# Optimization experiments

Hardware: AMD Instinct MI355X
Metric: run time of the kernel (lower is better)

## Reference

```python
import jax, jax.numpy as jnp
import numpy as np

B, T, D, H = 2, 2048, 1024, 16
HD = D // H
ALPHA = HD ** -0.5
EPS = 1e-5


def setup_inputs() -> dict:
    key = jax.random.key(0)
    ks = jax.random.split(key, 8)
    x = jax.random.normal(ks[0], (B, T, D), dtype=jnp.float32)
    # additive causal mask: 0 where allowed, -inf where disallowed
    causal = jnp.triu(jnp.ones((T, T), dtype=bool), k=1)
    attention_mask = jnp.where(causal, -jnp.inf, 0.0).astype(jnp.float32)
    rab = jax.random.normal(ks[1], (1, H, T, T), dtype=jnp.float32) * 0.02
    W_in = jax.random.normal(ks[2], (D, 4 * D), dtype=jnp.float32) * (D ** -0.5)
    b_in = jnp.zeros((4 * D,), dtype=jnp.float32)
    W_out = jax.random.normal(ks[3], (D, D), dtype=jnp.float32) * (D ** -0.5)
    b_out = jnp.zeros((D,), dtype=jnp.float32)
    ln_w = jnp.ones((D,), dtype=jnp.float32)
    ln_b = jnp.zeros((D,), dtype=jnp.float32)
    return {"x": x, "attention_mask": attention_mask, "rab": rab,
            "W_in": W_in, "b_in": b_in, "W_out": W_out, "b_out": b_out,
            "ln_w": ln_w, "ln_b": ln_b}


def _heads(t):  # [B,T,D] -> [B,H,T,HD]
    return t.reshape(B, T, H, HD).transpose(0, 2, 1, 3)


def _layernorm(t, w, b):
    mu = jnp.mean(t, axis=-1, keepdims=True)
    var = jnp.mean(jnp.square(t - mu), axis=-1, keepdims=True)
    return (t - mu) * jax.lax.rsqrt(var + EPS) * w + b


def reference(x, attention_mask, rab, W_in, b_in, W_out, b_out, ln_w, ln_b):
    h = jax.nn.silu(x @ W_in + b_in)                      # [B,T,4D]
    U, V, Q, K = jnp.split(h, 4, axis=-1)
    Qh, Kh, Vh = _heads(Q), _heads(K), _heads(V)
    logits = jnp.einsum('bhqd,bhkd->bhqk', Qh, Kh) * ALPHA
    logits = logits + rab + attention_mask[None, None]    # [B,H,T,T]
    # allowed counts from the additive mask (0 == allowed)
    allowed = (attention_mask == 0).astype(jnp.float32)   # [T,T]
    denom = jnp.clip(jnp.sum(allowed, axis=-1, keepdims=True), 1.0)  # [T,1]
    logits_safe = jnp.where(jnp.isinf(logits) & (logits < 0), -1e9, logits)
    attn = jax.nn.silu(logits_safe) / denom[None, None]
    AV = jnp.einsum('bhqk,bhkd->bhqd', attn, Vh)
    AV = AV.transpose(0, 2, 1, 3).reshape(B, T, D)
    y = (_layernorm(AV, ln_w, ln_b) * U) @ W_out + b_out
    return y
```

## Files before the change

### kernel.cpp

```cpp
#include <hip/hip_runtime.h>

#define BATCH 2
#define TSEQ 2048
#define DIM 1024
#define NH 16
#define HDIM 64
#define MROWS (BATCH * TSEQ)

typedef __attribute__((ext_vector_type(4))) float f32x4;
typedef __attribute__((ext_vector_type(8))) short short8;

__device__ __forceinline__ unsigned short f2bf(float f) {
    union { float f; unsigned int u; } x; x.f = f;
    unsigned int r = x.u + 0x7fffu + ((x.u >> 16) & 1u);
    return (unsigned short)(r >> 16);
}

__device__ __forceinline__ float silu_f(float v) {
    return v * __builtin_amdgcn_rcpf(1.f + __expf(-v));
}

__device__ __forceinline__ void gl_lds16(const void* g, void* l) {
    __builtin_amdgcn_global_load_lds(
        (const __attribute__((address_space(1))) void*)g,
        (__attribute__((address_space(3))) void*)l, 16, 0, 0);
}

__device__ __forceinline__ short8 rd_swz(const unsigned short* base, int row, int chunk) {
    const char* b = (const char*)base;
    return *(const short8*)(b + row * 128 + (((chunk ^ (row & 7)) << 4)));
}

__global__ __launch_bounds__(256) void k_convert(const float* __restrict__ in,
                                                 unsigned short* __restrict__ out,
                                                 int n4) {
    int i = blockIdx.x * 256 + threadIdx.x;
    if (i < n4) {
        float4 v = ((const float4*)in)[i];
        union { unsigned short s[4]; uint2 u; } o;
        o.s[0] = f2bf(v.x); o.s[1] = f2bf(v.y); o.s[2] = f2bf(v.z); o.s[3] = f2bf(v.w);
        ((uint2*)out)[i] = o.u;
    }
}

__global__ __launch_bounds__(256) void k_transpose(const float* __restrict__ in,
                                                   unsigned short* __restrict__ out,
                                                   int R, int C) {
    __shared__ float tile[32][33];
    int tx = threadIdx.x, ty = threadIdx.y;
    int c0 = blockIdx.x * 32, r0 = blockIdx.y * 32;
    #pragma unroll
    for (int i = 0; i < 32; i += 8)
        tile[ty + i][tx] = in[(size_t)(r0 + ty + i) * C + c0 + tx];
    __syncthreads();
    #pragma unroll
    for (int i = 0; i < 32; i += 8)
        out[(size_t)(c0 + ty + i) * R + r0 + tx] = f2bf(tile[tx][ty + i]);
}

__global__ __launch_bounds__(256) void k_transpose_bf16(const unsigned short* __restrict__ in,
                                                        unsigned short* __restrict__ out,
                                                        int R, int C) {
    __shared__ unsigned short t[64][66];
    int tx = threadIdx.x, ty = threadIdx.y;
    int c0 = blockIdx.x * 64, r0 = blockIdx.y * 64;
    #pragma unroll
    for (int i = 0; i < 64; i += 4)
        t[ty + i][tx] = in[(size_t)(r0 + ty + i) * C + c0 + tx];
    __syncthreads();
    #pragma unroll
    for (int i = 0; i < 64; i += 4)
        out[(size_t)(c0 + ty + i) * R + r0 + tx] = t[tx][ty + i];
}

template <int EPI>
__global__ __launch_bounds__(256) void k_gemm(
    const unsigned short* __restrict__ A, const unsigned short* __restrict__ Bt,
    int M, int N, int K, const float* __restrict__ bias,
    float* __restrict__ outU, unsigned short* __restrict__ outV,
    unsigned short* __restrict__ outQ, unsigned short* __restrict__ outK,
    float* __restrict__ outY)
{
    __shared__ __align__(16) unsigned short sA[128 * 32];
    __shared__ __align__(16) unsigned short sB[128 * 32];
    const int tid = threadIdx.x;
    const int bm = blockIdx.x, bn = blockIdx.y;
    const int row0 = bm * 128, col0 = bn * 128;
    const int lane = tid & 63, w = tid >> 6;
    const int wrow = (w >> 1) * 64, wcol = (w & 1) * 64;
    const int lr = lane & 15, lk = lane >> 4;

    f32x4 acc[4][4] = {};

    for (int k0 = 0; k0 < K; k0 += 32) {
        for (int c = tid; c < 512; c += 256) {
            int r = c >> 2, kc = c & 3;
            gl_lds16(A + (size_t)(row0 + r) * K + k0 + kc * 8, sA + c * 8);
            gl_lds16(Bt + (size_t)(col0 + r) * K + k0 + kc * 8, sB + c * 8);
        }
        __syncthreads();
        short8 af[4], bf[4];
        #pragma unroll
        for (int m = 0; m < 4; ++m)
            af[m] = *(const short8*)(sA + (wrow + m * 16 + lr) * 32 + lk * 8);
        #pragma unroll
        for (int n = 0; n < 4; ++n)
            bf[n] = *(const short8*)(sB + (wcol + n * 16 + lr) * 32 + lk * 8);
        #pragma unroll
        for (int m = 0; m < 4; ++m)
            #pragma unroll
            for (int n = 0; n < 4; ++n)
                acc[m][n] = __builtin_amdgcn_mfma_f32_16x16x32_bf16(af[m], bf[n], acc[m][n], 0, 0, 0);
        __syncthreads();
    }

    #pragma unroll
    for (int m = 0; m < 4; ++m) {
        #pragma unroll
        for (int n = 0; n < 4; ++n) {
            int cg = col0 + wcol + n * 16 + lr;
            float bv = bias[cg];
            #pragma unroll
            for (int j = 0; j < 4; ++j) {
                int rg = row0 + wrow + m * 16 + lk * 4 + j;
                float v = acc[m][n][j] + bv;
                if (EPI == 1) {
                    float s = silu_f(v);
                    int sec = cg >> 10, cc = cg & 1023;
                    size_t off = ((size_t)rg << 10) + cc;
                    if (sec == 0) outU[off] = s;
                    else if (sec == 1) outV[off] = f2bf(s);
                    else if (sec == 2) outQ[off] = f2bf(s * 0.125f);
                    else outK[off] = f2bf(s);
                } else {
                    outY[(size_t)rg * N + cg] = v;
                }
            }
        }
    }
}

__global__ __launch_bounds__(256, 4) void k_attn(
    const unsigned short* __restrict__ Qb,
    const unsigned short* __restrict__ Kb,
    const unsigned short* __restrict__ Vt,
    const float* __restrict__ rab,
    float* __restrict__ AV)
{
    __shared__ __align__(16) unsigned short sK[2][64 * 64];
    __shared__ __align__(16) unsigned short sVt[2][64 * 64];
    __shared__ __align__(16) unsigned short sP[64 * 64];

    const int tid = threadIdx.x;
    const int lane = tid & 63;
    const int w = tid >> 6;
    const int lr = lane & 15;
    const int lk = lane >> 4;

    const int bid = blockIdx.x;
    const int idx = bid & 255;
    const int g = bid >> 8;
    const int h = idx & 15;
    const int r_ = idx >> 4;
    const int bb = g >> 1;
    const int qt = (g & 1) ? (31 - r_) : r_;
    const int q0 = qt * 64;

    short8 qreg[2];
    #pragma unroll
    for (int ks = 0; ks < 2; ++ks)
        qreg[ks] = *(const short8*)(Qb + (((size_t)(bb * TSEQ + q0 + w * 16 + lr)) << 10)
                                     + h * 64 + ks * 32 + lk * 8);

    int qrow[4]; float invq[4];
    #pragma unroll
    for (int j = 0; j < 4; ++j) {
        qrow[j] = q0 + w * 16 + lk * 4 + j;
        invq[j] = 1.f / (float)(qrow[j] + 1);
    }

    f32x4 acc[4] = {};

    #define STAGE(buf, kt_) do {                                                      \
        int k0s = (kt_) * 64;                                                         \
        for (int c = tid; c < 512; c += 256) {                                        \
            int rr = c >> 3, kc = c & 7;                                              \
            int kcs = kc ^ (rr & 7);                                                  \
            gl_lds16(Kb + (((size_t)(bb * TSEQ + k0s + rr)) << 10) + h * 64 + kcs * 8,\
                     sK[buf] + c * 8);                                                \
            gl_lds16(Vt + (((size_t)(h * 64 + rr)) << 12) + bb * TSEQ + k0s + kcs * 8,\
                     sVt[buf] + c * 8);                                               \
        }                                                                             \
    } while (0)

    const float* rabh = rab + (size_t)h * TSEQ * TSEQ;

    STAGE(0, 0);
    float rvc[4][4];
    #pragma unroll
    for (int nt = 0; nt < 4; ++nt)
        #pragma unroll
        for (int j = 0; j < 4; ++j)
            rvc[nt][j] = rabh[(size_t)qrow[j] * TSEQ + nt * 16 + lr];
    __syncthreads();

    int cur = 0;
    for (int kt = 0; kt <= qt; ++kt) {
        const int k0 = kt * 64;
        const bool have_next = (kt < qt);
        if (have_next) STAGE(cur ^ 1, kt + 1);

        float rvn[4][4];
        if (have_next) {
            #pragma unroll
            for (int nt = 0; nt < 4; ++nt)
                #pragma unroll
                for (int j = 0; j < 4; ++j)
                    rvn[nt][j] = rabh[(size_t)qrow[j] * TSEQ + k0 + 64 + nt * 16 + lr];
        }

        f32x4 s[4] = {};
        #pragma unroll
        for (int ks = 0; ks < 2; ++ks) {
            #pragma unroll
            for (int nt = 0; nt < 4; ++nt)
                s[nt] = __builtin_amdgcn_mfma_f32_16x16x32_bf16(
                    qreg[ks], rd_swz(sK[cur], nt * 16 + lr, ks * 4 + lk), s[nt], 0, 0, 0);
        }

        const bool full = (kt < qt);
        char* pb = (char*)sP;
        #pragma unroll
        for (int nt = 0; nt < 4; ++nt) {
            int k = k0 + nt * 16 + lr;
            #pragma unroll
            for (int j = 0; j < 4; ++j) {
                int prow = w * 16 + lk * 4 + j;
                float v = s[nt][j] + rvc[nt][j];
                float pv = (full || k <= qrow[j]) ? silu_f(v) * invq[j] : 0.f;
                *(unsigned short*)(pb + prow * 128 + (((nt * 16 + lr) * 2) ^ ((prow & 7) << 4)))
                    = f2bf(pv);
            }
        }

        #pragma unroll
        for (int ks = 0; ks < 2; ++ks) {
            short8 ap = rd_swz(sP, w * 16 + lr, ks * 4 + lk);
            #pragma unroll
            for (int dt = 0; dt < 4; ++dt)
                acc[dt] = __builtin_amdgcn_mfma_f32_16x16x32_bf16(
                    ap, rd_swz(sVt[cur], dt * 16 + lr, ks * 4 + lk), acc[dt], 0, 0, 0);
        }

        if (have_next) {
            #pragma unroll
            for (int nt = 0; nt < 4; ++nt)
                #pragma unroll
                for (int j = 0; j < 4; ++j)
                    rvc[nt][j] = rvn[nt][j];
        }

        __syncthreads();
        cur ^= 1;
    }
    #undef STAGE

    #pragma unroll
    for (int dt = 0; dt < 4; ++dt)
        #pragma unroll
        for (int j = 0; j < 4; ++j)
            AV[(((size_t)(bb * TSEQ + qrow[j])) << 10) + h * 64 + dt * 16 + lr] = acc[dt][j];
}

__global__ __launch_bounds__(256) void k_ln(const float* __restrict__ AV,
                                            const float* __restrict__ U,
                                            const float* __restrict__ lnw,
                                            const float* __restrict__ lnb,
                                            unsigned short* __restrict__ z) {
    __shared__ float red[8];
    const int row = blockIdx.x, tid = threadIdx.x;
    float4 v = ((const float4*)(AV + ((size_t)row << 10)))[tid];
    float s = v.x + v.y + v.z + v.w;
    float s2 = v.x * v.x + v.y * v.y + v.z * v.z + v.w * v.w;
    #pragma unroll
    for (int o = 32; o > 0; o >>= 1) { s += __shfl_xor(s, o); s2 += __shfl_xor(s2, o); }
    const int w = tid >> 6;
    if ((tid & 63) == 0) { red[w] = s; red[4 + w] = s2; }
    __syncthreads();
    s = red[0] + red[1] + red[2] + red[3];
    s2 = red[4] + red[5] + red[6] + red[7];
    const float mu = s * (1.f / 1024.f);
    const float var = s2 * (1.f / 1024.f) - mu * mu;
    const float rstd = rsqrtf(var + 1e-5f);
    float4 uw = ((const float4*)(U + ((size_t)row << 10)))[tid];
    float4 lw = ((const float4*)lnw)[tid];
    float4 lb = ((const float4*)lnb)[tid];
    union { unsigned short o[4]; uint2 u; } ov;
    ov.o[0] = f2bf(((v.x - mu) * rstd * lw.x + lb.x) * uw.x);
    ov.o[1] = f2bf(((v.y - mu) * rstd * lw.y + lb.y) * uw.y);
    ov.o[2] = f2bf(((v.z - mu) * rstd * lw.z + lb.z) * uw.z);
    ov.o[3] = f2bf(((v.w - mu) * rstd * lw.w + lb.w) * uw.w);
    ((uint2*)z)[((size_t)row << 8) + tid] = ov.u;
}

extern "C" void kernel_launch(void* const* d_in, const int* in_sizes, int n_in,
                              void* d_out, int out_size, void* d_ws, size_t ws_size,
                              hipStream_t stream) {
    const float* x     = (const float*)d_in[0];
    const float* rab   = (const float*)d_in[2];
    const float* W_in  = (const float*)d_in[3];
    const float* b_in  = (const float*)d_in[4];
    const float* W_out = (const float*)d_in[5];
    const float* b_out = (const float*)d_in[6];
    const float* ln_w  = (const float*)d_in[7];
    const float* ln_b  = (const float*)d_in[8];
    float* y = (float*)d_out;

    char* ws = (char*)d_ws;
    size_t off = 0;
    auto alloc = [&](size_t bytes) -> void* {
        void* p = ws + off;
        off += (bytes + 255) & ~(size_t)255;
        return p;
    };
    unsigned short* WinT  = (unsigned short*)alloc((size_t)4096 * 1024 * 2);
    unsigned short* WoutT = (unsigned short*)alloc((size_t)1024 * 1024 * 2);
    unsigned short* xb    = (unsigned short*)alloc((size_t)MROWS * DIM * 2);
    float*          Ubuf  = (float*)alloc((size_t)MROWS * DIM * 4);
    unsigned short* Vb    = (unsigned short*)alloc((size_t)MROWS * DIM * 2);
    unsigned short* Qb    = (unsigned short*)alloc((size_t)MROWS * DIM * 2);
    unsigned short* Kb    = (unsigned short*)alloc((size_t)MROWS * DIM * 2);
    unsigned short* Vtb   = (unsigned short*)alloc((size_t)DIM * MROWS * 2);
    float*          AV    = (float*)alloc((size_t)MROWS * DIM * 4);
    unsigned short* z     = (unsigned short*)alloc((size_t)MROWS * DIM * 2);

    k_convert<<<dim3(4096), dim3(256), 0, stream>>>(x, xb, MROWS * DIM / 4);
    k_transpose<<<dim3(128, 32), dim3(32, 8), 0, stream>>>(W_in, WinT, 1024, 4096);
    k_transpose<<<dim3(32, 32), dim3(32, 8), 0, stream>>>(W_out, WoutT, 1024, 1024);
    k_gemm<1><<<dim3(32, 32), dim3(256), 0, stream>>>(xb, WinT, MROWS, 4096, 1024,
                                                      b_in, Ubuf, Vb, Qb, Kb, nullptr);
    k_transpose_bf16<<<dim3(16, 64), dim3(64, 4), 0, stream>>>(Vb, Vtb, MROWS, DIM);
    k_attn<<<dim3(1024), dim3(256), 0, stream>>>(Qb, Kb, Vtb, rab, AV);
    k_ln<<<dim3(MROWS), dim3(256), 0, stream>>>(AV, Ubuf, ln_w, ln_b, z);
    k_gemm<2><<<dim3(32, 8), dim3(256), 0, stream>>>(z, WoutT, MROWS, 1024, 1024,
                                                     b_out, nullptr, nullptr, nullptr, nullptr, y);
}
```

Before: 195.3 us.

## Write V transposed from GEMM epilogue, seed logits with rab, fold 1/(q+1) into LayerNorm eps

The input GEMM epilogue now writes V directly in transposed layout as packed 4-element stores, so the separate bf16 transpose kernel and the intermediate V buffer are removed. In attention, the rab tile is loaded straight into the MFMA accumulators as the initial value. The per-row 1/(q+1) scaling is dropped and compensated in LayerNorm by scaling eps by (q+1)^2, which relies on LayerNorm being invariant to row scaling. This removes a kernel launch, one global round trip for V, and some per-element multiplies, at the cost of strided transposed writes from the GEMM and a small change in the float rounding of P.

```diff
diff --git a/kernel.cpp b/kernel.cpp
--- a/kernel.cpp
+++ b/kernel.cpp
@@ -58,26 +58,11 @@
         out[(size_t)(c0 + ty + i) * R + r0 + tx] = f2bf(tile[tx][ty + i]);
 }
 
-__global__ __launch_bounds__(256) void k_transpose_bf16(const unsigned short* __restrict__ in,
-                                                        unsigned short* __restrict__ out,
-                                                        int R, int C) {
-    __shared__ unsigned short t[64][66];
-    int tx = threadIdx.x, ty = threadIdx.y;
-    int c0 = blockIdx.x * 64, r0 = blockIdx.y * 64;
-    #pragma unroll
-    for (int i = 0; i < 64; i += 4)
-        t[ty + i][tx] = in[(size_t)(r0 + ty + i) * C + c0 + tx];
-    __syncthreads();
-    #pragma unroll
-    for (int i = 0; i < 64; i += 4)
-        out[(size_t)(c0 + ty + i) * R + r0 + tx] = t[tx][ty + i];
-}
-
 template <int EPI>
 __global__ __launch_bounds__(256) void k_gemm(
     const unsigned short* __restrict__ A, const unsigned short* __restrict__ Bt,
     int M, int N, int K, const float* __restrict__ bias,
-    float* __restrict__ outU, unsigned short* __restrict__ outV,
+    float* __restrict__ outU, unsigned short* __restrict__ outVt,
     unsigned short* __restrict__ outQ, unsigned short* __restrict__ outK,
     float* __restrict__ outY)
 {
@@ -120,21 +105,35 @@
         for (int n = 0; n < 4; ++n) {
             int cg = col0 + wcol + n * 16 + lr;
             float bv = bias[cg];
-            #pragma unroll
-            for (int j = 0; j < 4; ++j) {
-                int rg = row0 + wrow + m * 16 + lk * 4 + j;
-                float v = acc[m][n][j] + bv;
-                if (EPI == 1) {
-                    float s = silu_f(v);
-                    int sec = cg >> 10, cc = cg & 1023;
-                    size_t off = ((size_t)rg << 10) + cc;
-                    if (sec == 0) outU[off] = s;
-                    else if (sec == 1) outV[off] = f2bf(s);
-                    else if (sec == 2) outQ[off] = f2bf(s * 0.125f);
-                    else outK[off] = f2bf(s);
+            int rg0 = row0 + wrow + m * 16 + lk * 4;
+            if (EPI == 1) {
+                float sv[4];
+                #pragma unroll
+                for (int j = 0; j < 4; ++j)
+                    sv[j] = silu_f(acc[m][n][j] + bv);
+                int sec = cg >> 10, cc = cg & 1023;
+                if (sec == 0) {
+                    #pragma unroll
+                    for (int j = 0; j < 4; ++j)
+                        outU[((size_t)(rg0 + j) << 10) + cc] = sv[j];
+                } else if (sec == 1) {
+                    union { unsigned short s[4]; uint2 u; } pk;
+                    #pragma unroll
+                    for (int j = 0; j < 4; ++j) pk.s[j] = f2bf(sv[j]);
+                    *(uint2*)(outVt + ((size_t)cc << 12) + rg0) = pk.u;
+                } else if (sec == 2) {
+                    #pragma unroll
+                    for (int j = 0; j < 4; ++j)
+                        outQ[((size_t)(rg0 + j) << 10) + cc] = f2bf(sv[j] * 0.125f);
                 } else {
-                    outY[(size_t)rg * N + cg] = v;
+                    #pragma unroll
+                    for (int j = 0; j < 4; ++j)
+                        outK[((size_t)(rg0 + j) << 10) + cc] = f2bf(sv[j]);
                 }
+            } else {
+                #pragma unroll
+                for (int j = 0; j < 4; ++j)
+                    outY[(size_t)(rg0 + j) * N + cg] = acc[m][n][j] + bv;
             }
         }
     }
@@ -172,11 +171,13 @@
         qreg[ks] = *(const short8*)(Qb + (((size_t)(bb * TSEQ + q0 + w * 16 + lr)) << 10)
                                      + h * 64 + ks * 32 + lk * 8);
 
-    int qrow[4]; float invq[4];
+    int qrow[4];
+    const float* rabrow[4];
+    const float* rabh = rab + (size_t)h * TSEQ * TSEQ;
     #pragma unroll
     for (int j = 0; j < 4; ++j) {
         qrow[j] = q0 + w * 16 + lk * 4 + j;
-        invq[j] = 1.f / (float)(qrow[j] + 1);
+        rabrow[j] = rabh + (size_t)qrow[j] * TSEQ + lr;
     }
 
     f32x4 acc[4] = {};
@@ -193,15 +194,13 @@
         }                                                                             \
     } while (0)
 
-    const float* rabh = rab + (size_t)h * TSEQ * TSEQ;
-
     STAGE(0, 0);
     float rvc[4][4];
     #pragma unroll
     for (int nt = 0; nt < 4; ++nt)
         #pragma unroll
         for (int j = 0; j < 4; ++j)
-            rvc[nt][j] = rabh[(size_t)qrow[j] * TSEQ + nt * 16 + lr];
+            rvc[nt][j] = rabrow[j][nt * 16];
     __syncthreads();
 
     int cur = 0;
@@ -216,10 +215,17 @@
             for (int nt = 0; nt < 4; ++nt)
                 #pragma unroll
                 for (int j = 0; j < 4; ++j)
-                    rvn[nt][j] = rabh[(size_t)qrow[j] * TSEQ + k0 + 64 + nt * 16 + lr];
-        }
-
-        f32x4 s[4] = {};
+                    rvn[nt][j] = rabrow[j][k0 + 64 + nt * 16];
+        }
+
+        f32x4 s[4];
+        #pragma unroll
+        for (int nt = 0; nt < 4; ++nt) {
+            f32x4 c0v;
+            c0v[0] = rvc[nt][0]; c0v[1] = rvc[nt][1];
+            c0v[2] = rvc[nt][2]; c0v[3] = rvc[nt][3];
+            s[nt] = c0v;
+        }
         #pragma unroll
         for (int ks = 0; ks < 2; ++ks) {
             #pragma unroll
@@ -231,15 +237,15 @@
         const bool full = (kt < qt);
         char* pb = (char*)sP;
         #pragma unroll
-        for (int nt = 0; nt < 4; ++nt) {
-            int k = k0 + nt * 16 + lr;
-            #pragma unroll
-            for (int j = 0; j < 4; ++j) {
-                int prow = w * 16 + lk * 4 + j;
-                float v = s[nt][j] + rvc[nt][j];
-                float pv = (full || k <= qrow[j]) ? silu_f(v) * invq[j] : 0.f;
-                *(unsigned short*)(pb + prow * 128 + (((nt * 16 + lr) * 2) ^ ((prow & 7) << 4)))
-                    = f2bf(pv);
+        for (int j = 0; j < 4; ++j) {
+            const int prow = w * 16 + lk * 4 + j;
+            char* bj = pb + prow * 128;
+            const int swz = ((lk * 4 + j) & 7) << 4;
+            #pragma unroll
+            for (int nt = 0; nt < 4; ++nt) {
+                int k = k0 + nt * 16 + lr;
+                float pv = (full || k <= qrow[j]) ? silu_f(s[nt][j]) : 0.f;
+                *(unsigned short*)(bj + (((nt << 5) | (lr << 1)) ^ swz)) = f2bf(pv);
             }
         }
 
@@ -279,6 +285,8 @@
                                             unsigned short* __restrict__ z) {
     __shared__ float red[8];
     const int row = blockIdx.x, tid = threadIdx.x;
+    const float c = (float)((row & (TSEQ - 1)) + 1);
+    const float eps = 1e-5f * c * c;
     float4 v = ((const float4*)(AV + ((size_t)row << 10)))[tid];
     float s = v.x + v.y + v.z + v.w;
     float s2 = v.x * v.x + v.y * v.y + v.z * v.z + v.w * v.w;
@@ -291,7 +299,7 @@
     s2 = red[4] + red[5] + red[6] + red[7];
     const float mu = s * (1.f / 1024.f);
     const float var = s2 * (1.f / 1024.f) - mu * mu;
-    const float rstd = rsqrtf(var + 1e-5f);
+    const float rstd = rsqrtf(var + eps);
     float4 uw = ((const float4*)(U + ((size_t)row << 10)))[tid];
     float4 lw = ((const float4*)lnw)[tid];
     float4 lb = ((const float4*)lnb)[tid];
@@ -327,7 +335,6 @@
     unsigned short* WoutT = (unsigned short*)alloc((size_t)1024 * 1024 * 2);
     unsigned short* xb    = (unsigned short*)alloc((size_t)MROWS * DIM * 2);
     float*          Ubuf  = (float*)alloc((size_t)MROWS * DIM * 4);
-    unsigned short* Vb    = (unsigned short*)alloc((size_t)MROWS * DIM * 2);
     unsigned short* Qb    = (unsigned short*)alloc((size_t)MROWS * DIM * 2);
     unsigned short* Kb    = (unsigned short*)alloc((size_t)MROWS * DIM * 2);
     unsigned short* Vtb   = (unsigned short*)alloc((size_t)DIM * MROWS * 2);
@@ -338,8 +345,7 @@
     k_transpose<<<dim3(128, 32), dim3(32, 8), 0, stream>>>(W_in, WinT, 1024, 4096);
     k_transpose<<<dim3(32, 32), dim3(32, 8), 0, stream>>>(W_out, WoutT, 1024, 1024);
     k_gemm<1><<<dim3(32, 32), dim3(256), 0, stream>>>(xb, WinT, MROWS, 4096, 1024,
-                                                      b_in, Ubuf, Vb, Qb, Kb, nullptr);
-    k_transpose_bf16<<<dim3(16, 64), dim3(64, 4), 0, stream>>>(Vb, Vtb, MROWS, DIM);
+                                                      b_in, Ubuf, Vtb, Qb, Kb, nullptr);
     k_attn<<<dim3(1024), dim3(256), 0, stream>>>(Qb, Kb, Vtb, rab, AV);
     k_ln<<<dim3(MROWS), dim3(256), 0, stream>>>(AV, Ubuf, ln_w, ln_b, z);
     k_gemm<2><<<dim3(32, 8), dim3(256), 0, stream>>>(z, WoutT, MROWS, 1024, 1024,
```

After: 186.4 us. -4.6%, faster.
